# Kernel tuning notes

Hardware: AMD Instinct MI355X
Metric: run time of the kernel (lower is better)

## Reference

```python
import jax, jax.numpy as jnp
import numpy as np

N_NODES = 50000
N_EDGES = 800000
D_IN, D_HID, D_LAT = 128, 128, 64
BN_EPS = 1e-5


def setup_inputs() -> dict:
    key = jax.random.key(0)
    ks = jax.random.split(key, 8)
    x = jax.random.normal(ks[0], (N_NODES, D_IN), dtype=jnp.float32)
    edge_index = jax.random.randint(ks[1], (2, N_EDGES), 0, N_NODES, dtype=jnp.int64)
    s1 = 1.0 / np.sqrt(D_IN)
    s2 = 1.0 / np.sqrt(D_HID)
    W1 = jax.random.normal(ks[2], (D_IN, D_HID), dtype=jnp.float32) * s1
    b1 = jnp.zeros((D_HID,), jnp.float32)
    gamma = jnp.ones((D_HID,), jnp.float32)
    beta = jnp.zeros((D_HID,), jnp.float32)
    Wmu = jax.random.normal(ks[3], (D_HID, D_LAT), dtype=jnp.float32) * s2
    bmu = jnp.zeros((D_LAT,), jnp.float32)
    Wls = jax.random.normal(ks[4], (D_HID, D_LAT), dtype=jnp.float32) * s2
    bls = jnp.zeros((D_LAT,), jnp.float32)
    return {"x": x, "edge_index": edge_index, "W1": W1, "b1": b1,
            "gamma": gamma, "beta": beta, "Wmu": Wmu, "bmu": bmu,
            "Wls": Wls, "bls": bls}


def _gcn_conv(h, src, dst, norm_e, inv_deg, W, b):
    # PyG GCNConv: linear transform, then sym-normalized aggregation (A+I).
    h = h @ W                                   # [N, F]
    msgs = h[src] * norm_e[:, None]             # gather + edge scaling, [E, F]
    agg = jax.ops.segment_sum(msgs, dst, num_segments=h.shape[0])
    # self-loop contribution: norm[i]*norm[i] = 1/deg[i]
    return agg + h * inv_deg[:, None] + b


def reference(x, edge_index, W1, b1, gamma, beta, Wmu, bmu, Wls, bls):
    src, dst = edge_index[0], edge_index[1]
    n = x.shape[0]
    # degrees including self loops (GCN symmetric normalization)
    deg = jax.ops.segment_sum(jnp.ones(dst.shape, x.dtype), dst, num_segments=n) + 1.0
    inv_sqrt_deg = jax.lax.rsqrt(deg)
    norm_e = inv_sqrt_deg[src] * inv_sqrt_deg[dst]   # per-edge norm, [E]
    inv_deg = 1.0 / deg

    h = _gcn_conv(x, src, dst, norm_e, inv_deg, W1, b1)
    # BatchNorm1d with batch statistics (biased var), then ReLU; dropout off (eval)
    mean = h.mean(axis=0)
    var = h.var(axis=0)
    h = (h - mean) * jax.lax.rsqrt(var + BN_EPS) * gamma + beta
    h = jax.nn.relu(h)

    mu = _gcn_conv(h, src, dst, norm_e, inv_deg, Wmu, bmu)
    log_std = _gcn_conv(h, src, dst, norm_e, inv_deg, Wls, bls)
    return mu, log_std
```

## Files before the change

### kernel.cpp

```cpp
#include <hip/hip_runtime.h>
#include <hip/hip_bf16.h>

#define N_NODES 50000
#define N_EDGES 800000
#define F 128
#define L 64
#define BN_EPS 1e-5f
#define SCAN_BLOCKS 196
#define BN_BLOCKS 391
#define EDGE_BLOCKS2 1563
#define GEMM_BLOCKS 782
#define NPART 8
#define PART_SZ 6250
#define SUBS_F 256
#define FILLB_A 2048

typedef __attribute__((ext_vector_type(8))) short short8;
typedef __attribute__((ext_vector_type(8))) unsigned short ushort8;
typedef __attribute__((ext_vector_type(4))) unsigned short ushortx4;
typedef __attribute__((ext_vector_type(4))) float f32x4;

static __device__ __forceinline__ float loadF(const void* p, int i, int f32) {
    if (f32) return ((const float*)p)[i];
    return __bfloat162float(((const __hip_bfloat16*)p)[i]);
}
static __device__ __forceinline__ float bfu2f(unsigned short u) {
    unsigned int t = ((unsigned int)u) << 16;
    float f;
    __builtin_memcpy(&f, &t, 4);
    return f;
}
static __device__ __forceinline__ short f2bf_s(float f) {
    union { __hip_bfloat16 b; short s; } cv;
    cv.b = __float2bfloat16(f);
    return cv.s;
}
static __device__ __forceinline__ unsigned short f2bf_u(float f) {
    union { __hip_bfloat16 b; unsigned short u; } cv;
    cv.b = __float2bfloat16(f);
    return cv.u;
}

__global__ void k_wprep(const void* __restrict__ W1, const void* __restrict__ Wmu,
                        const void* __restrict__ Wls, const unsigned short* __restrict__ xs,
                        const void* __restrict__ ei, __hip_bfloat16* __restrict__ Wt1,
                        __hip_bfloat16* __restrict__ Wt2, int* __restrict__ flags,
                        int* __restrict__ degi) {
    int b = blockIdx.x;
    int t = threadIdx.x;
    if (b == 0) {
        __shared__ int cnt[2];
        if (t < 2) cnt[t] = 0;
        __syncthreads();
        unsigned short v = xs[2 * t];
        int e = (v >> 7) & 0xff;
        int sane = (e >= 112 && e <= 133) ? 1 : 0;
        if (v == 0 || v == 0x8000) sane = 1;
        atomicAdd(&cnt[0], sane);
        atomicAdd(&cnt[1], (((const int*)ei)[2 * t + 1] != 0) ? 1 : 0);
        __syncthreads();
        if (t == 0) {
            flags[0] = (cnt[0] < 128) ? 1 : 0;
            flags[1] = (cnt[1] < 8) ? 1 : 0;
            flags[2] = 0;
        }
    } else if (b <= 64) {
        __shared__ int cnt;
        if (t == 0) cnt = 0;
        __syncthreads();
        unsigned short v = ((const unsigned short*)W1)[2 * t];
        int e = (v >> 7) & 0xff;
        atomicAdd(&cnt, (e >= 100 && e <= 133) ? 1 : 0);
        __syncthreads();
        int f32 = (cnt < 128) ? 1 : 0;
        int idx = (b - 1) * 256 + t;
        int n = idx >> 7, k = idx & 127;
        Wt1[idx] = __float2bfloat16(loadF(W1, k * F + n, f32));
        float v2 = (n < L) ? loadF(Wmu, k * L + n, f32) : loadF(Wls, k * L + (n - L), f32);
        Wt2[idx] = __float2bfloat16(v2);
    } else {
        int i = (b - 65) * 256 + t;
        if (i < 50048) degi[i] = 0;
    }
}

static __device__ __forceinline__ void gemm_body(int bid, const void* __restrict__ Xin,
        const __hip_bfloat16* __restrict__ Wt, const int* __restrict__ flags, int mode,
        const float* __restrict__ bnscale, const float* __restrict__ bnshift,
        const float* __restrict__ isd, unsigned short* __restrict__ outb) {
    int wave = threadIdx.x >> 6, lane = threadIdx.x & 63;
    int quad = lane >> 4, mr = lane & 15;
    int m0 = bid * 64 + wave * 16;
    int node = m0 + mr;
    int row = (node < N_NODES) ? node : N_NODES - 1;
    short8 a[4];
    if (mode == 1) {
        const unsigned short* xb = (const unsigned short*)Xin;
#pragma unroll
        for (int t = 0; t < 4; ++t) {
            int k0 = t * 32 + quad * 8;
            ushort8 raw = *(const ushort8*)(xb + row * F + k0);
            f32x4 s0 = *(const f32x4*)(bnscale + k0);
            f32x4 s1 = *(const f32x4*)(bnscale + k0 + 4);
            f32x4 h0 = *(const f32x4*)(bnshift + k0);
            f32x4 h1 = *(const f32x4*)(bnshift + k0 + 4);
            short8 av;
#pragma unroll
            for (int j = 0; j < 4; ++j)
                av[j] = f2bf_s(fmaxf(bfu2f(raw[j]) * s0[j] + h0[j], 0.f));
#pragma unroll
            for (int j = 0; j < 4; ++j)
                av[4 + j] = f2bf_s(fmaxf(bfu2f(raw[4 + j]) * s1[j] + h1[j], 0.f));
            a[t] = av;
        }
    } else if (flags[0]) {
        const float* xf = (const float*)Xin;
#pragma unroll
        for (int t = 0; t < 4; ++t) {
            int off = row * F + t * 32 + quad * 8;
            f32x4 v0 = *(const f32x4*)(xf + off);
            f32x4 v1 = *(const f32x4*)(xf + off + 4);
            short8 av;
#pragma unroll
            for (int j = 0; j < 4; ++j) av[j] = f2bf_s(v0[j]);
#pragma unroll
            for (int j = 0; j < 4; ++j) av[4 + j] = f2bf_s(v1[j]);
            a[t] = av;
        }
    } else {
        const short* xb = (const short*)Xin;
#pragma unroll
        for (int t = 0; t < 4; ++t)
            a[t] = *(const short8*)(xb + row * F + t * 32 + quad * 8);
    }
    f32x4 acc[8];
    const short* wb = (const short*)Wt;
#pragma unroll
    for (int nt = 0; nt < 8; ++nt) {
        const short* wp = wb + (nt * 16 + mr) * F + quad * 8;
        f32x4 c = {0.f, 0.f, 0.f, 0.f};
        c = __builtin_amdgcn_mfma_f32_16x16x32_bf16(*(const short8*)(wp), a[0], c, 0, 0, 0);
        c = __builtin_amdgcn_mfma_f32_16x16x32_bf16(*(const short8*)(wp + 32), a[1], c, 0, 0, 0);
        c = __builtin_amdgcn_mfma_f32_16x16x32_bf16(*(const short8*)(wp + 64), a[2], c, 0, 0, 0);
        c = __builtin_amdgcn_mfma_f32_16x16x32_bf16(*(const short8*)(wp + 96), a[3], c, 0, 0, 0);
        acc[nt] = c;
    }
    if (node < N_NODES) {
        float sd = (mode == 1) ? isd[node] : 1.0f;
        unsigned short* op = outb + node * F;
#pragma unroll
        for (int nt = 0; nt < 8; ++nt) {
            ushortx4 r;
#pragma unroll
            for (int j = 0; j < 4; ++j) r[j] = f2bf_u(acc[nt][j] * sd);
            *(ushortx4*)(op + nt * 16 + quad * 4) = r;
        }
    }
}

__global__ __launch_bounds__(256) void k_edge_gemm1(
        const void* __restrict__ X, const __hip_bfloat16* __restrict__ Wt1,
        const int* __restrict__ flags, const void* __restrict__ ei,
        int* __restrict__ degi, unsigned short* __restrict__ src16,
        unsigned short* __restrict__ dst16, unsigned short* __restrict__ rank16,
        unsigned short* __restrict__ outb) {
    if (blockIdx.x < GEMM_BLOCKS) {
        gemm_body(blockIdx.x, X, Wt1, flags, 0, nullptr, nullptr, nullptr, outb);
    } else {
        int t = threadIdx.x;
        int ebase = (blockIdx.x - GEMM_BLOCKS) * 512;
        __shared__ int nz;
        if (t == 0) nz = 0;
        __syncthreads();
        int e0 = ebase + t;
        if (e0 < N_EDGES) {
            int w = ((const int*)ei)[2 * e0 + 1];
            if (w != 0) atomicAdd(&nz, 1);
        }
        __syncthreads();
        int i64 = (nz < 8) ? 1 : 0;
#pragma unroll
        for (int k = 0; k < 2; ++k) {
            int e = ebase + k * 256 + t;
            if (e < N_EDGES) {
                int s, d;
                if (i64) {
                    s = (int)((const long long*)ei)[e];
                    d = (int)((const long long*)ei)[N_EDGES + e];
                } else {
                    s = ((const int*)ei)[e];
                    d = ((const int*)ei)[N_EDGES + e];
                }
                src16[e] = (unsigned short)s;
                dst16[e] = (unsigned short)d;
                rank16[e] = (unsigned short)atomicAdd(&degi[d], 1);
            }
        }
    }
}

__global__ void k_offs_alloc(const int* __restrict__ degi, int* __restrict__ flags,
                             int* __restrict__ offs, float* __restrict__ isd) {
    __shared__ int s[256];
    __shared__ int base;
    int t = threadIdx.x;
    int i = blockIdx.x * 256 + t;
    int v = (i < N_NODES) ? degi[i] : 0;
    s[t] = v;
    __syncthreads();
    for (int o = 1; o < 256; o <<= 1) {
        int u = (t >= o) ? s[t - o] : 0;
        __syncthreads();
        s[t] += u;
        __syncthreads();
    }
    if (t == 255) base = atomicAdd(&flags[2], s[255]);
    __syncthreads();
    if (i < N_NODES) {
        offs[i] = base + s[t] - v;
        isd[i] = 1.0f / sqrtf((float)v + 1.0f);
    }
}

__global__ __launch_bounds__(256) void k_fill(
        const unsigned short* __restrict__ src16, const unsigned short* __restrict__ dst16,
        const unsigned short* __restrict__ rank16, const int* __restrict__ offs,
        unsigned short* __restrict__ csr16) {
    int grp = blockIdx.x & (NPART - 1);
    int sub = blockIdx.x >> 3;
    int lo = grp * PART_SZ, hi = lo + PART_SZ;
    int stride = SUBS_F * 256;
    for (int e = sub * 256 + threadIdx.x; e < N_EDGES; e += stride) {
        int d = dst16[e];
        if (d >= lo && d < hi) csr16[offs[d] + rank16[e]] = src16[e];
    }
}

__global__ __launch_bounds__(256) void k_gemm_bn(const void* __restrict__ Xin,
        const __hip_bfloat16* __restrict__ Wt, const int* __restrict__ flags,
        const float* __restrict__ bnscale, const float* __restrict__ bnshift,
        const float* __restrict__ isd, unsigned short* __restrict__ outb) {
    gemm_body(blockIdx.x, Xin, Wt, flags, 1, bnscale, bnshift, isd, outb);
}

template <int USE_ISD>
static __device__ __forceinline__ void agg_accum(int node, int grp, int l16,
        const ushort8* __restrict__ vp, const unsigned short* __restrict__ csr,
        const int* __restrict__ offs, const int* __restrict__ degi,
        const float* __restrict__ isd, float acc[8]) {
#pragma unroll
    for (int j = 0; j < 8; ++j) acc[j] = 0.f;
    if (grp == 0) {
        ushort8 u = vp[node * 16 + l16];
        if (USE_ISD) {
            float w = isd[node];
#pragma unroll
            for (int j = 0; j < 8; ++j) acc[j] = bfu2f(u[j]) * w;
        } else {
#pragma unroll
            for (int j = 0; j < 8; ++j) acc[j] = bfu2f(u[j]);
        }
    }
    int start = offs[node];
    int deg = degi[node];
    int i = start + ((deg * grp) >> 2);
    int ge = start + ((deg * (grp + 1)) >> 2);
    for (; i + 3 < ge; i += 4) {
        int s0 = csr[i], s1 = csr[i + 1], s2 = csr[i + 2], s3 = csr[i + 3];
        ushort8 u0 = vp[s0 * 16 + l16];
        ushort8 u1 = vp[s1 * 16 + l16];
        ushort8 u2 = vp[s2 * 16 + l16];
        ushort8 u3 = vp[s3 * 16 + l16];
        if (USE_ISD) {
            float w0 = isd[s0], w1 = isd[s1], w2 = isd[s2], w3 = isd[s3];
#pragma unroll
            for (int j = 0; j < 8; ++j)
                acc[j] += (bfu2f(u0[j]) * w0 + bfu2f(u1[j]) * w1) +
                          (bfu2f(u2[j]) * w2 + bfu2f(u3[j]) * w3);
        } else {
#pragma unroll
            for (int j = 0; j < 8; ++j)
                acc[j] += (bfu2f(u0[j]) + bfu2f(u1[j])) + (bfu2f(u2[j]) + bfu2f(u3[j]));
        }
    }
    for (; i < ge; ++i) {
        int s0 = csr[i];
        ushort8 u = vp[s0 * 16 + l16];
        if (USE_ISD) {
            float w0 = isd[s0];
#pragma unroll
            for (int j = 0; j < 8; ++j) acc[j] += bfu2f(u[j]) * w0;
        } else {
#pragma unroll
            for (int j = 0; j < 8; ++j) acc[j] += bfu2f(u[j]);
        }
    }
#pragma unroll
    for (int j = 0; j < 8; ++j) {
        acc[j] += __shfl_xor(acc[j], 16);
        acc[j] += __shfl_xor(acc[j], 32);
    }
}

__global__ void k_agg1(const unsigned short* __restrict__ val,
                       const unsigned short* __restrict__ csr,
                       const int* __restrict__ offs, const int* __restrict__ degi,
                       const float* __restrict__ isd, const void* __restrict__ b1,
                       const int* __restrict__ flags, unsigned short* __restrict__ out) {
    int node = blockIdx.x * 4 + (threadIdx.x >> 6);
    if (node >= N_NODES) return;
    int lane = threadIdx.x & 63;
    int grp = lane >> 4, l16 = lane & 15;
    float acc[8];
    agg_accum<1>(node, grp, l16, (const ushort8*)val, csr, offs, degi, isd, acc);
    if (grp == 0) {
        float sd = isd[node];
        int c0 = l16 * 8, f32 = flags[0];
        ushort8 r;
#pragma unroll
        for (int j = 0; j < 8; ++j) r[j] = f2bf_u(acc[j] * sd + loadF(b1, c0 + j, f32));
        ((ushort8*)out)[node * 16 + l16] = r;
    }
}

__global__ void k_bnstats(const unsigned short* __restrict__ h, float* __restrict__ partial) {
    __shared__ float ls[256][8];
    __shared__ float lq[256][8];
    int t = threadIdx.x;
    int o = t & 15, rg = t >> 4;
    int row0 = blockIdx.x * 128 + rg;
    float s[8] = {0.f}, q[8] = {0.f};
#pragma unroll
    for (int i = 0; i < 8; ++i) {
        int row = row0 + i * 16;
        if (row < N_NODES) {
            ushort8 u = *(const ushort8*)(h + row * F + o * 8);
#pragma unroll
            for (int j = 0; j < 8; ++j) {
                float v = bfu2f(u[j]);
                s[j] += v;
                q[j] += v * v;
            }
        }
    }
#pragma unroll
    for (int j = 0; j < 8; ++j) { ls[t][j] = s[j]; lq[t][j] = q[j]; }
    __syncthreads();
    if (t < 128) {
        int c = t, oo = c >> 3, jj = c & 7;
        float ts = 0.f, tq = 0.f;
#pragma unroll
        for (int rgi = 0; rgi < 16; ++rgi) {
            ts += ls[rgi * 16 + oo][jj];
            tq += lq[rgi * 16 + oo][jj];
        }
        partial[blockIdx.x * 256 + c] = ts;
        partial[blockIdx.x * 256 + 128 + c] = tq;
    }
}

__global__ void k_bnredprep(const float* __restrict__ partial, const void* __restrict__ gamma,
                            const void* __restrict__ beta, const int* __restrict__ flags,
                            float* __restrict__ scale, float* __restrict__ shift) {
    int c = blockIdx.x;
    float s = 0.f, q = 0.f;
    for (int b = threadIdx.x; b < BN_BLOCKS; b += 256) {
        s += partial[b * 256 + c];
        q += partial[b * 256 + 128 + c];
    }
#pragma unroll
    for (int o = 32; o; o >>= 1) {
        s += __shfl_down(s, o);
        q += __shfl_down(q, o);
    }
    __shared__ float ws[4], wq[4];
    if ((threadIdx.x & 63) == 0) {
        ws[threadIdx.x >> 6] = s;
        wq[threadIdx.x >> 6] = q;
    }
    __syncthreads();
    if (threadIdx.x == 0) {
        float S = ws[0] + ws[1] + ws[2] + ws[3];
        float Q = wq[0] + wq[1] + wq[2] + wq[3];
        const float invN = 1.0f / (float)N_NODES;
        float m = S * invN;
        float var = Q * invN - m * m;
        int f32 = flags[0];
        float sc = loadF(gamma, c, f32) * rsqrtf(var + BN_EPS);
        scale[c] = sc;
        shift[c] = loadF(beta, c, f32) - m * sc;
    }
}

__global__ void k_agg2(const unsigned short* __restrict__ val,
                       const unsigned short* __restrict__ csr,
                       const int* __restrict__ offs, const int* __restrict__ degi,
                       const float* __restrict__ isd, const void* __restrict__ bmu,
                       const void* __restrict__ bls, const int* __restrict__ flags,
                       void* __restrict__ out) {
    int node = blockIdx.x * 4 + (threadIdx.x >> 6);
    if (node >= N_NODES) return;
    int lane = threadIdx.x & 63;
    int grp = lane >> 4, l16 = lane & 15;
    float acc[8];
    agg_accum<0>(node, grp, l16, (const ushort8*)val, csr, offs, degi, isd, acc);
    if (grp == 0) {
        float sd = isd[node];
        int c0 = l16 * 8, f32 = flags[0];
        int hsel = (c0 >= L) ? 1 : 0;
        int cc = c0 - hsel * L;
        const void* bp = hsel ? bls : bmu;
        float o8[8];
#pragma unroll
        for (int j = 0; j < 8; ++j) o8[j] = acc[j] * sd + loadF(bp, cc + j, f32);
        long base_o = (long)hsel * (N_NODES * 64) + (long)node * 64 + cc;
        if (f32) {
            f32x4 r0 = {o8[0], o8[1], o8[2], o8[3]};
            f32x4 r1 = {o8[4], o8[5], o8[6], o8[7]};
            __builtin_nontemporal_store(r0, (f32x4*)((float*)out + base_o));
            __builtin_nontemporal_store(r1, (f32x4*)((float*)out + base_o + 4));
        } else {
            ushort8 r;
#pragma unroll
            for (int j = 0; j < 8; ++j) r[j] = f2bf_u(o8[j]);
            __builtin_nontemporal_store(r, (ushort8*)((__hip_bfloat16*)out + base_o));
        }
    }
}

extern "C" void kernel_launch(void* const* d_in, const int* in_sizes, int n_in,
                              void* d_out, int out_size, void* d_ws, size_t ws_size,
                              hipStream_t stream) {
    const void* x     = d_in[0];
    const void* ei    = d_in[1];
    const void* W1    = d_in[2];
    const void* b1    = d_in[3];
    const void* gamma = d_in[4];
    const void* beta  = d_in[5];
    const void* Wmu   = d_in[6];
    const void* bmu   = d_in[7];
    const void* Wls   = d_in[8];
    const void* bls   = d_in[9];

    int*   degi  = (int*)d_ws;
    int*   offs  = degi + 50048;
    float* isd   = (float*)(offs + 50048);
    float* stats = isd + 50048;
    int*   flags = (int*)(stats + 512);
    unsigned short* csr16  = (unsigned short*)(flags + 16);
    unsigned short* src16  = csr16 + 800000;
    unsigned short* dst16  = src16 + 800000;
    unsigned short* rank16 = dst16 + 800000;
    __hip_bfloat16* Wt1 = (__hip_bfloat16*)(rank16 + 800000);
    __hip_bfloat16* Wt2 = Wt1 + 16384;
    unsigned short* Abf = (unsigned short*)(Wt2 + 16384);
    unsigned short* Hpre = Abf + N_NODES * F;
    float* partial = (float*)(Hpre + N_NODES * F);

    const int NT = 256;
    const int AGG_BLOCKS = (N_NODES + 3) / 4;

    k_wprep<<<65 + SCAN_BLOCKS, NT, 0, stream>>>(W1, Wmu, Wls, (const unsigned short*)x,
                                                 ei, Wt1, Wt2, flags, degi);
    k_edge_gemm1<<<GEMM_BLOCKS + EDGE_BLOCKS2, NT, 0, stream>>>(
        x, Wt1, flags, ei, degi, src16, dst16, rank16, Abf);
    k_offs_alloc<<<SCAN_BLOCKS, NT, 0, stream>>>(degi, flags, offs, isd);
    k_fill<<<FILLB_A, NT, 0, stream>>>(src16, dst16, rank16, offs, csr16);
    k_agg1<<<AGG_BLOCKS, NT, 0, stream>>>(Abf, csr16, offs, degi, isd, b1, flags, Hpre);
    k_bnstats<<<BN_BLOCKS, NT, 0, stream>>>(Hpre, partial);
    k_bnredprep<<<128, NT, 0, stream>>>(partial, gamma, beta, flags, stats, stats + 128);
    k_gemm_bn<<<GEMM_BLOCKS, NT, 0, stream>>>(Hpre, Wt2, flags, stats, stats + 128,
                                              isd, Abf);
    k_agg2<<<AGG_BLOCKS, NT, 0, stream>>>(Abf, csr16, offs, degi, isd, bmu, bls, flags, d_out);
}
```

Baseline: 270.4 us.

## Fuse BatchNorm statistics into first aggregation kernel with grid-stride loop

The first GCN aggregation kernel becomes a persistent grid-stride kernel that also accumulates per-channel sum and sum of squares in registers, writing per-block partials. This removes the separate BN statistics pass that re-read the whole hidden activation. BN stats are now computed from fp32 values before bf16 rounding, which differs slightly from the old path. The degree-buffer zeroing moves from extra blocks of the weight-prep kernel to a hipMemsetAsync, and the partial reduction now covers 2048 blocks instead of 391.

```diff
diff --git a/kernel.cpp b/kernel.cpp
--- a/kernel.cpp
+++ b/kernel.cpp
@@ -7,13 +7,13 @@
 #define L 64
 #define BN_EPS 1e-5f
 #define SCAN_BLOCKS 196
-#define BN_BLOCKS 391
 #define EDGE_BLOCKS2 1563
 #define GEMM_BLOCKS 782
 #define NPART 8
 #define PART_SZ 6250
 #define SUBS_F 256
 #define FILLB_A 2048
+#define AGB 2048
 
 typedef __attribute__((ext_vector_type(8))) short short8;
 typedef __attribute__((ext_vector_type(8))) unsigned short ushort8;
@@ -44,8 +44,7 @@
 __global__ void k_wprep(const void* __restrict__ W1, const void* __restrict__ Wmu,
                         const void* __restrict__ Wls, const unsigned short* __restrict__ xs,
                         const void* __restrict__ ei, __hip_bfloat16* __restrict__ Wt1,
-                        __hip_bfloat16* __restrict__ Wt2, int* __restrict__ flags,
-                        int* __restrict__ degi) {
+                        __hip_bfloat16* __restrict__ Wt2, int* __restrict__ flags) {
     int b = blockIdx.x;
     int t = threadIdx.x;
     if (b == 0) {
@@ -64,7 +63,7 @@
             flags[1] = (cnt[1] < 8) ? 1 : 0;
             flags[2] = 0;
         }
-    } else if (b <= 64) {
+    } else {
         __shared__ int cnt;
         if (t == 0) cnt = 0;
         __syncthreads();
@@ -78,9 +77,6 @@
         Wt1[idx] = __float2bfloat16(loadF(W1, k * F + n, f32));
         float v2 = (n < L) ? loadF(Wmu, k * L + n, f32) : loadF(Wls, k * L + (n - L), f32);
         Wt2[idx] = __float2bfloat16(v2);
-    } else {
-        int i = (b - 65) * 256 + t;
-        if (i < 50048) degi[i] = 0;
     }
 }
 
@@ -302,60 +298,49 @@
     }
 }
 
-__global__ void k_agg1(const unsigned short* __restrict__ val,
-                       const unsigned short* __restrict__ csr,
-                       const int* __restrict__ offs, const int* __restrict__ degi,
-                       const float* __restrict__ isd, const void* __restrict__ b1,
-                       const int* __restrict__ flags, unsigned short* __restrict__ out) {
-    int node = blockIdx.x * 4 + (threadIdx.x >> 6);
-    if (node >= N_NODES) return;
+__global__ void k_agg1s(const unsigned short* __restrict__ val,
+                        const unsigned short* __restrict__ csr,
+                        const int* __restrict__ offs, const int* __restrict__ degi,
+                        const float* __restrict__ isd, const void* __restrict__ b1,
+                        const int* __restrict__ flags, unsigned short* __restrict__ out,
+                        float* __restrict__ partial) {
+    int wv = threadIdx.x >> 6;
     int lane = threadIdx.x & 63;
     int grp = lane >> 4, l16 = lane & 15;
-    float acc[8];
-    agg_accum<1>(node, grp, l16, (const ushort8*)val, csr, offs, degi, isd, acc);
+    int f32 = flags[0];
+    float sreg[8] = {0.f, 0.f, 0.f, 0.f, 0.f, 0.f, 0.f, 0.f};
+    float qreg[8] = {0.f, 0.f, 0.f, 0.f, 0.f, 0.f, 0.f, 0.f};
+    for (int node = blockIdx.x * 4 + wv; node < N_NODES; node += AGB * 4) {
+        float acc[8];
+        agg_accum<1>(node, grp, l16, (const ushort8*)val, csr, offs, degi, isd, acc);
+        if (grp == 0) {
+            float sd = isd[node];
+            int c0 = l16 * 8;
+            ushort8 r;
+#pragma unroll
+            for (int j = 0; j < 8; ++j) {
+                float v = acc[j] * sd + loadF(b1, c0 + j, f32);
+                r[j] = f2bf_u(v);
+                sreg[j] += v;
+                qreg[j] += v * v;
+            }
+            ((ushort8*)out)[node * 16 + l16] = r;
+        }
+    }
+    __shared__ float ls[4][128];
+    __shared__ float lq[4][128];
     if (grp == 0) {
-        float sd = isd[node];
-        int c0 = l16 * 8, f32 = flags[0];
-        ushort8 r;
-#pragma unroll
-        for (int j = 0; j < 8; ++j) r[j] = f2bf_u(acc[j] * sd + loadF(b1, c0 + j, f32));
-        ((ushort8*)out)[node * 16 + l16] = r;
-    }
-}
-
-__global__ void k_bnstats(const unsigned short* __restrict__ h, float* __restrict__ partial) {
-    __shared__ float ls[256][8];
-    __shared__ float lq[256][8];
+        int c0 = l16 * 8;
+#pragma unroll
+        for (int j = 0; j < 8; ++j) { ls[wv][c0 + j] = sreg[j]; lq[wv][c0 + j] = qreg[j]; }
+    }
+    __syncthreads();
     int t = threadIdx.x;
-    int o = t & 15, rg = t >> 4;
-    int row0 = blockIdx.x * 128 + rg;
-    float s[8] = {0.f}, q[8] = {0.f};
-#pragma unroll
-    for (int i = 0; i < 8; ++i) {
-        int row = row0 + i * 16;
-        if (row < N_NODES) {
-            ushort8 u = *(const ushort8*)(h + row * F + o * 8);
-#pragma unroll
-            for (int j = 0; j < 8; ++j) {
-                float v = bfu2f(u[j]);
-                s[j] += v;
-                q[j] += v * v;
-            }
-        }
-    }
-#pragma unroll
-    for (int j = 0; j < 8; ++j) { ls[t][j] = s[j]; lq[t][j] = q[j]; }
-    __syncthreads();
     if (t < 128) {
-        int c = t, oo = c >> 3, jj = c & 7;
-        float ts = 0.f, tq = 0.f;
-#pragma unroll
-        for (int rgi = 0; rgi < 16; ++rgi) {
-            ts += ls[rgi * 16 + oo][jj];
-            tq += lq[rgi * 16 + oo][jj];
-        }
-        partial[blockIdx.x * 256 + c] = ts;
-        partial[blockIdx.x * 256 + 128 + c] = tq;
+        float s = ls[0][t] + ls[1][t] + ls[2][t] + ls[3][t];
+        float q = lq[0][t] + lq[1][t] + lq[2][t] + lq[3][t];
+        partial[blockIdx.x * 256 + t] = s;
+        partial[blockIdx.x * 256 + 128 + t] = q;
     }
 }
 
@@ -364,7 +349,7 @@
                             float* __restrict__ scale, float* __restrict__ shift) {
     int c = blockIdx.x;
     float s = 0.f, q = 0.f;
-    for (int b = threadIdx.x; b < BN_BLOCKS; b += 256) {
+    for (int b = threadIdx.x; b < AGB; b += 256) {
         s += partial[b * 256 + c];
         q += partial[b * 256 + 128 + c];
     }
@@ -460,14 +445,15 @@
     const int NT = 256;
     const int AGG_BLOCKS = (N_NODES + 3) / 4;
 
-    k_wprep<<<65 + SCAN_BLOCKS, NT, 0, stream>>>(W1, Wmu, Wls, (const unsigned short*)x,
-                                                 ei, Wt1, Wt2, flags, degi);
+    hipMemsetAsync(degi, 0, 50048 * sizeof(int), stream);
+    k_wprep<<<65, NT, 0, stream>>>(W1, Wmu, Wls, (const unsigned short*)x, ei,
+                                   Wt1, Wt2, flags);
     k_edge_gemm1<<<GEMM_BLOCKS + EDGE_BLOCKS2, NT, 0, stream>>>(
         x, Wt1, flags, ei, degi, src16, dst16, rank16, Abf);
     k_offs_alloc<<<SCAN_BLOCKS, NT, 0, stream>>>(degi, flags, offs, isd);
     k_fill<<<FILLB_A, NT, 0, stream>>>(src16, dst16, rank16, offs, csr16);
-    k_agg1<<<AGG_BLOCKS, NT, 0, stream>>>(Abf, csr16, offs, degi, isd, b1, flags, Hpre);
-    k_bnstats<<<BN_BLOCKS, NT, 0, stream>>>(Hpre, partial);
+    k_agg1s<<<AGB, NT, 0, stream>>>(Abf, csr16, offs, degi, isd, b1, flags,
+                                    Hpre, partial);
     k_bnredprep<<<128, NT, 0, stream>>>(partial, gamma, beta, flags, stats, stats + 128);
     k_gemm_bn<<<GEMM_BLOCKS, NT, 0, stream>>>(Hpre, Wt2, flags, stats, stats + 128,
                                               isd, Abf);
```

New measurement: 288.3 us. +6.6%, slower.
